# Kernel tuning notes

Measured on AMD Instinct MI355X. Metric: run time of the kernel, lower is better.

## Reference

```python
import jax, jax.numpy as jnp
import numpy as np
import math

GROUPS = 32
EPS = 1e-5
N_HEADS = 8  # channels=512 / num_head_channels=64


def group_norm(x, w, b):
    # x: [B, C, T]; GroupNorm over (channels-in-group, T)
    B, C, T = x.shape
    xg = x.reshape(B, GROUPS, C // GROUPS * T)
    mu = xg.mean(axis=-1, keepdims=True)
    var = xg.var(axis=-1, keepdims=True)
    xn = ((xg - mu) * jax.lax.rsqrt(var + EPS)).reshape(B, C, T)
    return xn * w[None, :, None] + b[None, :, None]


def setup_inputs() -> dict:
    key = jax.random.key(0)
    ks = jax.random.split(key, 7)
    C = 512
    return {
        "x": jax.random.normal(ks[0], (8, C, 32, 32), dtype=jnp.float32),
        "norm_w": jax.random.normal(ks[1], (C,), dtype=jnp.float32),
        "norm_b": jax.random.normal(ks[2], (C,), dtype=jnp.float32),
        "qkv_w": jax.random.normal(ks[3], (3 * C, C), dtype=jnp.float32) * 0.02,
        "qkv_b": jax.random.normal(ks[4], (3 * C,), dtype=jnp.float32) * 0.02,
        "proj_w": jax.random.normal(ks[5], (C, C), dtype=jnp.float32) * 0.02,
        "proj_b": jax.random.normal(ks[6], (C,), dtype=jnp.float32) * 0.02,
    }


def reference(x, norm_w, norm_b, qkv_w, qkv_b, proj_w, proj_b):
    b, c, H, W = x.shape
    T = H * W
    xf = x.reshape(b, c, T)
    xn = group_norm(xf, norm_w, norm_b)
    # 1x1 conv1d == channel matmul: [3C, C] x [B, C, T] -> [B, 3C, T]
    qkv = jnp.einsum('oc,bct->bot', qkv_w, xn) + qkv_b[None, :, None]
    ch = c // N_HEADS
    qkv = qkv.reshape(b * N_HEADS, 3 * ch, T)
    q, k, v = qkv[:, :ch], qkv[:, ch:2 * ch], qkv[:, 2 * ch:]
    scale = 1.0 / math.sqrt(math.sqrt(ch))
    # [BH, T, T] score matrix (explicit, as in the original)
    weight = jnp.einsum('bct,bcs->bts', q * scale, k * scale)
    weight = jax.nn.softmax(weight.astype(jnp.float32), axis=-1).astype(qkv.dtype)
    a = jnp.einsum('bts,bcs->bct', weight, v).reshape(b, c, T)
    hout = jnp.einsum('oc,bct->bot', proj_w, a) + proj_b[None, :, None]
    return (xf + hout).reshape(b, c, H, W)
```

## Files before the change

### kernel.cpp

```cpp
#include <hip/hip_runtime.h>
#include <math.h>

typedef float f32x4_t __attribute__((ext_vector_type(4)));
typedef short bf16x8_t __attribute__((ext_vector_type(8)));

#define B_   8
#define C_   512
#define T_   1024
#define NH_  8
#define CH_  64
#define EPSF 1e-5f

#define MFMA16(a, b, c) __builtin_amdgcn_mfma_f32_16x16x32_bf16((a), (b), (c), 0, 0, 0)

#define GLD16(gp, lp) __builtin_amdgcn_global_load_lds( \
    (const __attribute__((address_space(1))) unsigned int*)(gp), \
    (__attribute__((address_space(3))) unsigned int*)(lp), 16, 0, 0)

__device__ __forceinline__ unsigned short f2bf(float f) {
  union { float f; unsigned u; } v; v.f = f;
  unsigned r = v.u + 0x7FFFu + ((v.u >> 16) & 1u);
  return (unsigned short)(r >> 16);
}

__global__ __launch_bounds__(256) void prep_gn_kernel(
    const float* __restrict__ x, const float* __restrict__ w,
    const float* __restrict__ bvec, unsigned short* __restrict__ xnT,
    const float* __restrict__ qw_f, const float* __restrict__ pw_f,
    unsigned short* __restrict__ qw, unsigned short* __restrict__ pw)
{
  __shared__ __align__(16) float xs[16 * 1024];
  __shared__ float rs_[4], r2_[4];
  __shared__ float mu_s, rsig_s;

  int tid = threadIdx.x;
  if (blockIdx.x >= 256) {
    int idx = (blockIdx.x - 256) * 256 + tid;
    const int N1 = 1536 * 512 / 4;
    const int N2 = 512 * 512 / 4;
    if (idx < N1) {
      float4 v = ((const float4*)qw_f)[idx];
      uint2 o;
      o.x = (unsigned)f2bf(v.x) | ((unsigned)f2bf(v.y) << 16);
      o.y = (unsigned)f2bf(v.z) | ((unsigned)f2bf(v.w) << 16);
      ((uint2*)qw)[idx] = o;
    } else if (idx < N1 + N2) {
      int j = idx - N1;
      float4 v = ((const float4*)pw_f)[j];
      uint2 o;
      o.x = (unsigned)f2bf(v.x) | ((unsigned)f2bf(v.y) << 16);
      o.y = (unsigned)f2bf(v.z) | ((unsigned)f2bf(v.w) << 16);
      ((uint2*)pw)[j] = o;
    }
    return;
  }

  int blk = blockIdx.x;
  int b = blk >> 5, g = blk & 31;
  const float* xp = x + ((size_t)(b * C_ + g * 16)) * T_;
  const int N = 16 * T_;

  float s = 0.f, s2 = 0.f;
  for (int i = tid * 4; i < N; i += 256 * 4) {
    float4 v = *(const float4*)(xp + i);
    *(float4*)&xs[i] = v;
    s  += v.x + v.y + v.z + v.w;
    s2 += v.x * v.x + v.y * v.y + v.z * v.z + v.w * v.w;
  }
  for (int off = 32; off; off >>= 1) {
    s  += __shfl_down(s,  off, 64);
    s2 += __shfl_down(s2, off, 64);
  }
  int wid = tid >> 6, lane = tid & 63;
  if (lane == 0) { rs_[wid] = s; r2_[wid] = s2; }
  __syncthreads();
  if (tid == 0) {
    float ts = rs_[0] + rs_[1] + rs_[2] + rs_[3];
    float t2 = r2_[0] + r2_[1] + r2_[2] + r2_[3];
    float mu = ts / (float)N;
    float var = t2 / (float)N - mu * mu;
    mu_s = mu;
    rsig_s = rsqrtf(var + EPSF);
  }
  __syncthreads();
  float mu = mu_s, rs = rsig_s;

  float wl[16], bl[16];
  for (int c = 0; c < 16; ++c) { wl[c] = w[g * 16 + c]; bl[c] = bvec[g * 16 + c]; }

  for (int t = tid; t < T_; t += 256) {
    unsigned short buf[16] __attribute__((aligned(16)));
    for (int c = 0; c < 16; ++c) {
      float val = xs[c * T_ + t];
      buf[c] = f2bf((val - mu) * rs * wl[c] + bl[c]);
    }
    unsigned short* dst = xnT + ((size_t)b * T_ + t) * C_ + g * 16;
    *(uint4*)dst       = *(uint4*)buf;
    *(uint4*)(dst + 8) = *(uint4*)(buf + 8);
  }
}

__global__ __launch_bounds__(256) void gemm_qkv_kernel(
    const unsigned short* __restrict__ W, const unsigned short* __restrict__ xnT,
    const float* __restrict__ bias,
    unsigned short* __restrict__ q_t, unsigned short* __restrict__ k_t,
    unsigned short* __restrict__ v_c)
{
  int b = blockIdx.z;
  int m0 = blockIdx.y * 128, n0 = blockIdx.x * 128;
  int tid = threadIdx.x;
  int w = tid >> 6, lane = tid & 63, quad = lane >> 4, lr = lane & 15;
  int wm = w >> 1, wn = w & 1;

  __shared__ __align__(16) unsigned short Asl[2][128][32];
  __shared__ __align__(16) unsigned short Bsl[2][128][32];

  f32x4_t acc[4][4];
  for (int i = 0; i < 4; ++i)
    for (int j = 0; j < 4; ++j) acc[i][j] = (f32x4_t){0.f, 0.f, 0.f, 0.f};

  int ur = tid >> 2, uk = (tid & 3) * 8;
  const unsigned short* Ap = W + (size_t)(m0 + ur) * C_ + uk;
  const unsigned short* Bp = xnT + ((size_t)b * T_ + n0 + ur) * C_ + uk;

#define STAGE_QKV(buf, k0)                                        \
  do {                                                            \
    GLD16(Ap + (k0),            &Asl[buf][w * 16][0]);            \
    GLD16(Ap + 64 * C_ + (k0),  &Asl[buf][64 + w * 16][0]);       \
    GLD16(Bp + (k0),            &Bsl[buf][w * 16][0]);            \
    GLD16(Bp + 64 * C_ + (k0),  &Bsl[buf][64 + w * 16][0]);       \
  } while (0)

  STAGE_QKV(0, 0);
  __syncthreads();

  int cur = 0;
  for (int k0 = 0; k0 < C_; k0 += 32) {
    if (k0 + 32 < C_) STAGE_QKV(cur ^ 1, k0 + 32);
    bf16x8_t af[4], bfv[4];
    for (int i = 0; i < 4; ++i) af[i]  = *(bf16x8_t*)&Asl[cur][wm * 64 + i * 16 + lr][quad * 8];
    for (int j = 0; j < 4; ++j) bfv[j] = *(bf16x8_t*)&Bsl[cur][wn * 64 + j * 16 + lr][quad * 8];
    for (int i = 0; i < 4; ++i)
      for (int j = 0; j < 4; ++j)
        acc[i][j] = MFMA16(af[i], bfv[j], acc[i][j]);
    __syncthreads();
    cur ^= 1;
  }
#undef STAGE_QKV

  for (int i = 0; i < 4; ++i) {
    int ob = m0 + wm * 64 + i * 16 + quad * 4;
    int h = ob / 192, r0 = ob % 192;
    for (int j = 0; j < 4; ++j) {
      int t = n0 + wn * 64 + j * 16 + lr;
      if (r0 < 128) {
        unsigned short pk[4] __attribute__((aligned(8)));
      #pragma unroll
        for (int r = 0; r < 4; ++r) pk[r] = f2bf(acc[i][j][r] + bias[ob + r]);
        unsigned short* base = (r0 < 64) ? q_t : k_t;
        int chn = (r0 < 64) ? r0 : r0 - 64;
        *(uint2*)&base[((size_t)(b * NH_ + h) * T_ + t) * CH_ + chn] = *(uint2*)pk;
      } else {
      #pragma unroll
        for (int r = 0; r < 4; ++r) {
          float vv = acc[i][j][r] + bias[ob + r];
          v_c[((size_t)(b * NH_ + h) * CH_ + (r0 - 128 + r)) * T_ + t] = f2bf(vv);
        }
      }
    }
  }
}

__global__ __launch_bounds__(256) void attn_kernel(
    const unsigned short* __restrict__ q_t, const unsigned short* __restrict__ k_t,
    const unsigned short* __restrict__ v_c, unsigned short* __restrict__ a_t)
{
  int bh = blockIdx.x;
  int t0 = blockIdx.y * 128;
  int tid = threadIdx.x;
  int w = tid >> 6, lane = tid & 63, quad = lane >> 4, lr = lane & 15;

  __shared__ __align__(16) unsigned short q_s[128][72];
  __shared__ __align__(16) unsigned short p_s[128][72];
  __shared__ __align__(16) unsigned short k_s[64][72];
  __shared__ __align__(16) unsigned short v_s[64][72];

  int r0 = tid >> 3, c0 = (tid & 7) * 8;
#pragma unroll
  for (int cch = 0; cch < 4; ++cch)
    *(uint4*)&q_s[r0 + 32 * cch][c0] =
        *(const uint4*)&q_t[((size_t)bh * T_ + t0 + r0 + 32 * cch) * CH_ + c0];

  uint4 kr0 = *(const uint4*)&k_t[((size_t)bh * T_ + r0) * CH_ + c0];
  uint4 kr1 = *(const uint4*)&k_t[((size_t)bh * T_ + r0 + 32) * CH_ + c0];
  uint4 vr0 = *(const uint4*)&v_c[((size_t)bh * CH_ + r0) * T_ + c0];
  uint4 vr1 = *(const uint4*)&v_c[((size_t)bh * CH_ + r0 + 32) * T_ + c0];

  __syncthreads();
  bf16x8_t bq[2][2];
#pragma unroll
  for (int rb = 0; rb < 2; ++rb) {
    bq[rb][0] = *(bf16x8_t*)&q_s[w * 32 + rb * 16 + lr][quad * 8];
    bq[rb][1] = *(bf16x8_t*)&q_s[w * 32 + rb * 16 + lr][32 + quad * 8];
  }

  f32x4_t o_acc[2][4];
#pragma unroll
  for (int rb = 0; rb < 2; ++rb)
    for (int j = 0; j < 4; ++j) o_acc[rb][j] = (f32x4_t){0.f, 0.f, 0.f, 0.f};
  float l_sum[2] = {0.f, 0.f};

  const float SCL = 0.18033688f;
  const float MSH = 11.541560f;

  for (int s0 = 0; s0 < T_; s0 += 64) {
    __syncthreads();
    *(uint4*)&k_s[r0][c0]      = kr0;
    *(uint4*)&k_s[r0 + 32][c0] = kr1;
    *(uint4*)&v_s[r0][c0]      = vr0;
    *(uint4*)&v_s[r0 + 32][c0] = vr1;
    if (s0 + 64 < T_) {
      kr0 = *(const uint4*)&k_t[((size_t)bh * T_ + s0 + 64 + r0) * CH_ + c0];
      kr1 = *(const uint4*)&k_t[((size_t)bh * T_ + s0 + 96 + r0) * CH_ + c0];
      vr0 = *(const uint4*)&v_c[((size_t)bh * CH_ + r0) * T_ + s0 + 64 + c0];
      vr1 = *(const uint4*)&v_c[((size_t)bh * CH_ + r0 + 32) * T_ + s0 + 64 + c0];
    }
    __syncthreads();

    f32x4_t sc[4][2];
    __builtin_amdgcn_s_setprio(1);
#pragma unroll
    for (int j = 0; j < 4; ++j) {
      bf16x8_t ak0 = *(bf16x8_t*)&k_s[j * 16 + lr][quad * 8];
      bf16x8_t ak1 = *(bf16x8_t*)&k_s[j * 16 + lr][32 + quad * 8];
      f32x4_t a0 = (f32x4_t){0.f, 0.f, 0.f, 0.f};
      f32x4_t a1 = (f32x4_t){0.f, 0.f, 0.f, 0.f};
      a0 = MFMA16(ak0, bq[0][0], a0);
      a0 = MFMA16(ak1, bq[0][1], a0);
      a1 = MFMA16(ak0, bq[1][0], a1);
      a1 = MFMA16(ak1, bq[1][1], a1);
      sc[j][0] = a0;
      sc[j][1] = a1;
    }
    __builtin_amdgcn_s_setprio(0);

#pragma unroll
    for (int rb = 0; rb < 2; ++rb) {
      float rsum = 0.f;
#pragma unroll
      for (int j = 0; j < 4; ++j) {
        unsigned u[4];
#pragma unroll
        for (int r = 0; r < 4; ++r) {
          union { float f; unsigned v; } cv;
          cv.f = __builtin_amdgcn_exp2f(sc[j][rb][r] * SCL - MSH);
          u[r] = cv.v & 0xFFFF0000u;
          union { unsigned v; float f; } rf; rf.v = u[r];
          rsum += rf.f;
        }
        uint2 pk;
        pk.x = (u[0] >> 16) | u[1];
        pk.y = (u[2] >> 16) | u[3];
        *(uint2*)&p_s[w * 32 + rb * 16 + lr][j * 16 + quad * 4] = pk;
      }
      rsum += __shfl_xor(rsum, 16, 64);
      rsum += __shfl_xor(rsum, 32, 64);
      l_sum[rb] += rsum;
    }

    bf16x8_t ap[2][2];
#pragma unroll
    for (int rb = 0; rb < 2; ++rb) {
      ap[rb][0] = *(bf16x8_t*)&p_s[w * 32 + rb * 16 + lr][quad * 8];
      ap[rb][1] = *(bf16x8_t*)&p_s[w * 32 + rb * 16 + lr][32 + quad * 8];
    }

    __builtin_amdgcn_s_setprio(1);
#pragma unroll
    for (int j = 0; j < 4; ++j)
#pragma unroll
      for (int kk = 0; kk < 2; ++kk) {
        bf16x8_t bv = *(bf16x8_t*)&v_s[j * 16 + lr][kk * 32 + quad * 8];
        o_acc[0][j] = MFMA16(ap[0][kk], bv, o_acc[0][j]);
        o_acc[1][j] = MFMA16(ap[1][kk], bv, o_acc[1][j]);
      }
    __builtin_amdgcn_s_setprio(0);
  }

#pragma unroll
  for (int rb = 0; rb < 2; ++rb) {
#pragma unroll
    for (int r = 0; r < 4; ++r) {
      float lv = __shfl(l_sum[rb], quad * 4 + r, 64);
      float inv = 1.f / lv;
#pragma unroll
      for (int j = 0; j < 4; ++j)
        q_s[w * 32 + rb * 16 + quad * 4 + r][j * 16 + lr] = f2bf(o_acc[rb][j][r] * inv);
    }
  }
  __syncthreads();
#pragma unroll
  for (int cch = 0; cch < 4; ++cch)
    *(uint4*)&a_t[((size_t)bh * T_ + t0 + r0 + 32 * cch) * CH_ + c0] =
        *(uint4*)&q_s[r0 + 32 * cch][c0];
}

__global__ __launch_bounds__(256) void gemm_proj_kernel(
    const unsigned short* __restrict__ W, const unsigned short* __restrict__ a_t,
    const float* __restrict__ bias, const float* __restrict__ xres,
    float* __restrict__ out)
{
  int b = blockIdx.z;
  int m0 = blockIdx.y * 128, n0 = blockIdx.x * 128;
  int tid = threadIdx.x;
  int w = tid >> 6, lane = tid & 63, quad = lane >> 4, lr = lane & 15;
  int wm = w >> 1, wn = w & 1;

  __shared__ __align__(16) unsigned short Asl[2][128][32];
  __shared__ __align__(16) unsigned short Bsl[2][128][32];

  f32x4_t acc[4][4];
  for (int i = 0; i < 4; ++i)
    for (int j = 0; j < 4; ++j) acc[i][j] = (f32x4_t){0.f, 0.f, 0.f, 0.f};

  int ur = tid >> 2, uk = (tid & 3) * 8;
  const unsigned short* Ap = W + (size_t)(m0 + ur) * C_ + uk;

#define STAGE_PROJ(buf, k0)                                                   \
  do {                                                                        \
    const unsigned short* Bp = a_t +                                          \
        ((size_t)(b * NH_ + ((k0) >> 6)) * T_ + n0 + ur) * CH_ + ((k0) & 63) + uk; \
    GLD16(Ap + (k0),           &Asl[buf][w * 16][0]);                         \
    GLD16(Ap + 64 * C_ + (k0), &Asl[buf][64 + w * 16][0]);                    \
    GLD16(Bp,                  &Bsl[buf][w * 16][0]);                         \
    GLD16(Bp + 64 * CH_,       &Bsl[buf][64 + w * 16][0]);                    \
  } while (0)

  STAGE_PROJ(0, 0);
  __syncthreads();

  int cur = 0;
  for (int k0 = 0; k0 < C_; k0 += 32) {
    if (k0 + 32 < C_) STAGE_PROJ(cur ^ 1, k0 + 32);
    bf16x8_t af[4], bfv[4];
    for (int i = 0; i < 4; ++i) af[i]  = *(bf16x8_t*)&Asl[cur][wm * 64 + i * 16 + lr][quad * 8];
    for (int j = 0; j < 4; ++j) bfv[j] = *(bf16x8_t*)&Bsl[cur][wn * 64 + j * 16 + lr][quad * 8];
    for (int i = 0; i < 4; ++i)
      for (int j = 0; j < 4; ++j)
        acc[i][j] = MFMA16(af[i], bfv[j], acc[i][j]);
    __syncthreads();
    cur ^= 1;
  }
#undef STAGE_PROJ

  for (int i = 0; i < 4; ++i) {
    int ob = m0 + wm * 64 + i * 16 + quad * 4;
    for (int j = 0; j < 4; ++j) {
      int t = n0 + wn * 64 + j * 16 + lr;
    #pragma unroll
      for (int r = 0; r < 4; ++r) {
        size_t idx = ((size_t)(b * C_ + ob + r)) * T_ + t;
        out[idx] = acc[i][j][r] + bias[ob + r] + xres[idx];
      }
    }
  }
}

extern "C" void kernel_launch(void* const* d_in, const int* in_sizes, int n_in,
                              void* d_out, int out_size, void* d_ws, size_t ws_size,
                              hipStream_t stream)
{
  const float* x      = (const float*)d_in[0];
  const float* norm_w = (const float*)d_in[1];
  const float* norm_b = (const float*)d_in[2];
  const float* qkv_w  = (const float*)d_in[3];
  const float* qkv_b  = (const float*)d_in[4];
  const float* proj_w = (const float*)d_in[5];
  const float* proj_b = (const float*)d_in[6];
  float* out = (float*)d_out;

  char* ws = (char*)d_ws;
  unsigned short* qw  = (unsigned short*)ws;
  unsigned short* pw  = (unsigned short*)(ws + 1572864);
  unsigned short* xnT = (unsigned short*)(ws + 2097152);
  unsigned short* q_t = (unsigned short*)(ws + 10485760);
  unsigned short* k_t = (unsigned short*)(ws + 18874368);
  unsigned short* v_c = (unsigned short*)(ws + 27262976);
  unsigned short* a_t = (unsigned short*)(ws + 35651584);

  prep_gn_kernel<<<dim3(256 + 1024), dim3(256), 0, stream>>>(
      x, norm_w, norm_b, xnT, qkv_w, proj_w, qw, pw);

  gemm_qkv_kernel<<<dim3(T_ / 128, 1536 / 128, B_), dim3(256), 0, stream>>>(
      qw, xnT, qkv_b, q_t, k_t, v_c);

  attn_kernel<<<dim3(B_ * NH_, T_ / 128), dim3(256), 0, stream>>>(q_t, k_t, v_c, a_t);

  gemm_proj_kernel<<<dim3(T_ / 128, C_ / 128, B_), dim3(256), 0, stream>>>(
      pw, a_t, proj_b, x, out);
}
```

Before: 162.6 us.

## Load Q and V fragments directly from global into MFMA registers

The attention kernel no longer stages Q and V through shared memory. Q fragments are read straight from global memory into registers once per block. V fragments are loaded per tile directly into MFMA operand registers, which cuts LDS use and removes the V stores into shared memory. The softmax exponentials are folded into the score-MFMA loop, and the cross-lane row-sum shuffles are deferred to the end of the loop. The trade-off is that V loads are no longer prefetched a tile ahead, so their global latency has to be hidden behind the QK MFMAs within the same iteration.

```diff
diff --git a/kernel.cpp b/kernel.cpp
--- a/kernel.cpp
+++ b/kernel.cpp
@@ -180,29 +180,23 @@
   int tid = threadIdx.x;
   int w = tid >> 6, lane = tid & 63, quad = lane >> 4, lr = lane & 15;
 
-  __shared__ __align__(16) unsigned short q_s[128][72];
+  __shared__ __align__(16) unsigned short k_s[64][72];
   __shared__ __align__(16) unsigned short p_s[128][72];
-  __shared__ __align__(16) unsigned short k_s[64][72];
-  __shared__ __align__(16) unsigned short v_s[64][72];
 
   int r0 = tid >> 3, c0 = (tid & 7) * 8;
-#pragma unroll
-  for (int cch = 0; cch < 4; ++cch)
-    *(uint4*)&q_s[r0 + 32 * cch][c0] =
-        *(const uint4*)&q_t[((size_t)bh * T_ + t0 + r0 + 32 * cch) * CH_ + c0];
+
+  bf16x8_t bq[2][2];
+#pragma unroll
+  for (int rb = 0; rb < 2; ++rb)
+#pragma unroll
+    for (int kk = 0; kk < 2; ++kk)
+      bq[rb][kk] = *(const bf16x8_t*)
+          &q_t[((size_t)bh * T_ + t0 + w * 32 + rb * 16 + lr) * CH_ + kk * 32 + quad * 8];
 
   uint4 kr0 = *(const uint4*)&k_t[((size_t)bh * T_ + r0) * CH_ + c0];
   uint4 kr1 = *(const uint4*)&k_t[((size_t)bh * T_ + r0 + 32) * CH_ + c0];
-  uint4 vr0 = *(const uint4*)&v_c[((size_t)bh * CH_ + r0) * T_ + c0];
-  uint4 vr1 = *(const uint4*)&v_c[((size_t)bh * CH_ + r0 + 32) * T_ + c0];
-
-  __syncthreads();
-  bf16x8_t bq[2][2];
-#pragma unroll
-  for (int rb = 0; rb < 2; ++rb) {
-    bq[rb][0] = *(bf16x8_t*)&q_s[w * 32 + rb * 16 + lr][quad * 8];
-    bq[rb][1] = *(bf16x8_t*)&q_s[w * 32 + rb * 16 + lr][32 + quad * 8];
-  }
+
+  const unsigned short* vbase = v_c + ((size_t)bh * CH_ + lr) * T_ + quad * 8;
 
   f32x4_t o_acc[2][4];
 #pragma unroll
@@ -217,18 +211,19 @@
     __syncthreads();
     *(uint4*)&k_s[r0][c0]      = kr0;
     *(uint4*)&k_s[r0 + 32][c0] = kr1;
-    *(uint4*)&v_s[r0][c0]      = vr0;
-    *(uint4*)&v_s[r0 + 32][c0] = vr1;
+    __syncthreads();
     if (s0 + 64 < T_) {
       kr0 = *(const uint4*)&k_t[((size_t)bh * T_ + s0 + 64 + r0) * CH_ + c0];
       kr1 = *(const uint4*)&k_t[((size_t)bh * T_ + s0 + 96 + r0) * CH_ + c0];
-      vr0 = *(const uint4*)&v_c[((size_t)bh * CH_ + r0) * T_ + s0 + 64 + c0];
-      vr1 = *(const uint4*)&v_c[((size_t)bh * CH_ + r0 + 32) * T_ + s0 + 64 + c0];
-    }
-    __syncthreads();
-
-    f32x4_t sc[4][2];
-    __builtin_amdgcn_s_setprio(1);
+    }
+
+    bf16x8_t bvv[4][2];
+#pragma unroll
+    for (int j = 0; j < 4; ++j)
+#pragma unroll
+      for (int kk = 0; kk < 2; ++kk)
+        bvv[j][kk] = *(const bf16x8_t*)(vbase + (size_t)j * 16 * T_ + s0 + kk * 32);
+
 #pragma unroll
     for (int j = 0; j < 4; ++j) {
       bf16x8_t ak0 = *(bf16x8_t*)&k_s[j * 16 + lr][quad * 8];
@@ -239,21 +234,15 @@
       a0 = MFMA16(ak1, bq[0][1], a0);
       a1 = MFMA16(ak0, bq[1][0], a1);
       a1 = MFMA16(ak1, bq[1][1], a1);
-      sc[j][0] = a0;
-      sc[j][1] = a1;
-    }
-    __builtin_amdgcn_s_setprio(0);
-
-#pragma unroll
-    for (int rb = 0; rb < 2; ++rb) {
-      float rsum = 0.f;
-#pragma unroll
-      for (int j = 0; j < 4; ++j) {
+#pragma unroll
+      for (int rb = 0; rb < 2; ++rb) {
+        const f32x4_t& av = rb ? a1 : a0;
         unsigned u[4];
+        float rsum = 0.f;
 #pragma unroll
         for (int r = 0; r < 4; ++r) {
           union { float f; unsigned v; } cv;
-          cv.f = __builtin_amdgcn_exp2f(sc[j][rb][r] * SCL - MSH);
+          cv.f = __builtin_amdgcn_exp2f(av[r] * SCL - MSH);
           u[r] = cv.v & 0xFFFF0000u;
           union { unsigned v; float f; } rf; rf.v = u[r];
           rsum += rf.f;
@@ -262,10 +251,11 @@
         pk.x = (u[0] >> 16) | u[1];
         pk.y = (u[2] >> 16) | u[3];
         *(uint2*)&p_s[w * 32 + rb * 16 + lr][j * 16 + quad * 4] = pk;
+        l_sum[rb] += rsum;
       }
-      rsum += __shfl_xor(rsum, 16, 64);
-      rsum += __shfl_xor(rsum, 32, 64);
-      l_sum[rb] += rsum;
+    }
+#pragma unroll
+    for (int rb = 0; rb < 2; ++rb) {
     }
 
     bf16x8_t ap[2][2];
@@ -280,11 +270,16 @@
     for (int j = 0; j < 4; ++j)
 #pragma unroll
       for (int kk = 0; kk < 2; ++kk) {
-        bf16x8_t bv = *(bf16x8_t*)&v_s[j * 16 + lr][kk * 32 + quad * 8];
-        o_acc[0][j] = MFMA16(ap[0][kk], bv, o_acc[0][j]);
-        o_acc[1][j] = MFMA16(ap[1][kk], bv, o_acc[1][j]);
+        o_acc[0][j] = MFMA16(ap[0][kk], bvv[j][kk], o_acc[0][j]);
+        o_acc[1][j] = MFMA16(ap[1][kk], bvv[j][kk], o_acc[1][j]);
       }
     __builtin_amdgcn_s_setprio(0);
+  }
+
+#pragma unroll
+  for (int rb = 0; rb < 2; ++rb) {
+    l_sum[rb] += __shfl_xor(l_sum[rb], 16, 64);
+    l_sum[rb] += __shfl_xor(l_sum[rb], 32, 64);
   }
 
 #pragma unroll
@@ -295,14 +290,14 @@
       float inv = 1.f / lv;
 #pragma unroll
       for (int j = 0; j < 4; ++j)
-        q_s[w * 32 + rb * 16 + quad * 4 + r][j * 16 + lr] = f2bf(o_acc[rb][j][r] * inv);
+        p_s[w * 32 + rb * 16 + quad * 4 + r][j * 16 + lr] = f2bf(o_acc[rb][j][r] * inv);
     }
   }
   __syncthreads();
 #pragma unroll
   for (int cch = 0; cch < 4; ++cch)
     *(uint4*)&a_t[((size_t)bh * T_ + t0 + r0 + 32 * cch) * CH_ + c0] =
-        *(uint4*)&q_s[r0 + 32 * cch][c0];
+        *(uint4*)&p_s[r0 + 32 * cch][c0];
 }
 
 __global__ __launch_bounds__(256) void gemm_proj_kernel(
```

Result: slower. 166.9 us (+2.7%).

## Triple-buffer QKV and projection GEMM loads with one barrier per k-step

Applied to the files above, without the earlier changes.

Both channel GEMMs move from double-buffered LDS staging with two __syncthreads per iteration to a three-stage ring. Loads are issued two k-steps ahead, with an explicit vmcnt wait and a single s_barrier per iteration, so global-to-LDS loads overlap more with MFMA work. The attention softmax loop is also split so the row-sum is recomputed in a separate pass that re-evaluates exp2, which adds duplicated transcendental work. This leaves dead code behind. The extra LDS buffer raises shared memory use per block, which can lower occupancy.

```diff
diff --git a/kernel.cpp b/kernel.cpp
--- a/kernel.cpp
+++ b/kernel.cpp
@@ -112,8 +112,8 @@
   int w = tid >> 6, lane = tid & 63, quad = lane >> 4, lr = lane & 15;
   int wm = w >> 1, wn = w & 1;
 
-  __shared__ __align__(16) unsigned short Asl[2][128][32];
-  __shared__ __align__(16) unsigned short Bsl[2][128][32];
+  __shared__ __align__(16) unsigned short Asl[3][128][32];
+  __shared__ __align__(16) unsigned short Bsl[3][128][32];
 
   f32x4_t acc[4][4];
   for (int i = 0; i < 4; ++i)
@@ -132,19 +132,21 @@
   } while (0)
 
   STAGE_QKV(0, 0);
-  __syncthreads();
-
-  int cur = 0;
-  for (int k0 = 0; k0 < C_; k0 += 32) {
-    if (k0 + 32 < C_) STAGE_QKV(cur ^ 1, k0 + 32);
+  STAGE_QKV(1, 32);
+
+  for (int it = 0; it < 16; ++it) {
+    if (it < 15) asm volatile("s_waitcnt vmcnt(4)" ::: "memory");
+    else         asm volatile("s_waitcnt vmcnt(0)" ::: "memory");
+    __builtin_amdgcn_s_barrier();
+    __builtin_amdgcn_sched_barrier(0);
+    if (it + 2 < 16) STAGE_QKV((it + 2) % 3, (it + 2) * 32);
+    int cur = it % 3;
     bf16x8_t af[4], bfv[4];
     for (int i = 0; i < 4; ++i) af[i]  = *(bf16x8_t*)&Asl[cur][wm * 64 + i * 16 + lr][quad * 8];
     for (int j = 0; j < 4; ++j) bfv[j] = *(bf16x8_t*)&Bsl[cur][wn * 64 + j * 16 + lr][quad * 8];
     for (int i = 0; i < 4; ++i)
       for (int j = 0; j < 4; ++j)
         acc[i][j] = MFMA16(af[i], bfv[j], acc[i][j]);
-    __syncthreads();
-    cur ^= 1;
   }
 #undef STAGE_QKV
 
@@ -262,6 +264,22 @@
         pk.x = (u[0] >> 16) | u[1];
         pk.y = (u[2] >> 16) | u[3];
         *(uint2*)&p_s[w * 32 + rb * 16 + lr][j * 16 + quad * 4] = pk;
+        rsum = rsum;
+      }
+      (void)rsum;
+    }
+#pragma unroll
+    for (int rb = 0; rb < 2; ++rb) {
+      float rsum = 0.f;
+#pragma unroll
+      for (int j = 0; j < 4; ++j) {
+#pragma unroll
+        for (int r = 0; r < 4; ++r) {
+          union { float f; unsigned v; } cv;
+          cv.f = __builtin_amdgcn_exp2f(sc[j][rb][r] * SCL - MSH);
+          union { unsigned v; float f; } rf; rf.v = cv.v & 0xFFFF0000u;
+          rsum += rf.f;
+        }
       }
       rsum += __shfl_xor(rsum, 16, 64);
       rsum += __shfl_xor(rsum, 32, 64);
@@ -316,8 +334,8 @@
   int w = tid >> 6, lane = tid & 63, quad = lane >> 4, lr = lane & 15;
   int wm = w >> 1, wn = w & 1;
 
-  __shared__ __align__(16) unsigned short Asl[2][128][32];
-  __shared__ __align__(16) unsigned short Bsl[2][128][32];
+  __shared__ __align__(16) unsigned short Asl[3][128][32];
+  __shared__ __align__(16) unsigned short Bsl[3][128][32];
 
   f32x4_t acc[4][4];
   for (int i = 0; i < 4; ++i)
@@ -337,19 +355,21 @@
   } while (0)
 
   STAGE_PROJ(0, 0);
-  __syncthreads();
-
-  int cur = 0;
-  for (int k0 = 0; k0 < C_; k0 += 32) {
-    if (k0 + 32 < C_) STAGE_PROJ(cur ^ 1, k0 + 32);
+  STAGE_PROJ(1, 32);
+
+  for (int it = 0; it < 16; ++it) {
+    if (it < 15) asm volatile("s_waitcnt vmcnt(4)" ::: "memory");
+    else         asm volatile("s_waitcnt vmcnt(0)" ::: "memory");
+    __builtin_amdgcn_s_barrier();
+    __builtin_amdgcn_sched_barrier(0);
+    if (it + 2 < 16) STAGE_PROJ((it + 2) % 3, (it + 2) * 32);
+    int cur = it % 3;
     bf16x8_t af[4], bfv[4];
     for (int i = 0; i < 4; ++i) af[i]  = *(bf16x8_t*)&Asl[cur][wm * 64 + i * 16 + lr][quad * 8];
     for (int j = 0; j < 4; ++j) bfv[j] = *(bf16x8_t*)&Bsl[cur][wn * 64 + j * 16 + lr][quad * 8];
     for (int i = 0; i < 4; ++i)
       for (int j = 0; j < 4; ++j)
         acc[i][j] = MFMA16(af[i], bfv[j], acc[i][j]);
-    __syncthreads();
-    cur ^= 1;
   }
 #undef STAGE_PROJ
 
```

Result: faster. 150.2 us (median of 2 runs) (-7.7%).
